# Optimization experiments

Hardware: AMD Instinct MI355X
Metric: run time of the kernel (lower is better)

## Reference

```python
import jax, jax.numpy as jnp
import numpy as np

EPS = 1e-5
NUM_HEADS = 8
KEY_DIM = 32
V_DIM = 128  # att_ratio * key_dim

def bn2d(x, g, b, m, v):
    # inference BatchNorm2d on NCHW
    s = g * jax.lax.rsqrt(v + EPS)
    return x * s[None, :, None, None] + (b - m * s)[None, :, None, None]

def conv1x1(x, w):
    # w: [out_c, in_c], x: [B,C,H,W]
    return jnp.einsum('oc,bchw->bohw', w, x)

def _bn_params(key, c):
    k1, k2, k3, k4 = jax.random.split(key, 4)
    g = jax.random.uniform(k1, (c,), jnp.float32, 0.5, 1.5)
    b = jax.random.normal(k2, (c,), jnp.float32) * 0.1
    m = jax.random.normal(k3, (c,), jnp.float32) * 0.1
    v = jax.random.uniform(k4, (c,), jnp.float32, 0.5, 1.5)
    return g, b, m, v

def setup_inputs() -> dict:
    key = jax.random.key(0)
    ks = jax.random.split(key, 12)
    inp_dim, out_dim = 256, 512
    kv_out = (KEY_DIM + V_DIM) * NUM_HEADS      # 1280
    q_out = KEY_DIM * NUM_HEADS                 # 256
    merge_dim = V_DIM * NUM_HEADS               # 1024
    hid = out_dim * 2                            # mlp_ratio=2 -> 1024
    d = {}
    d['x'] = jax.random.normal(ks[0], (32, inp_dim, 32, 32), jnp.float32)
    d['kv_w'] = jax.random.normal(ks[1], (kv_out, inp_dim), jnp.float32) * 0.02
    d['kv_g'], d['kv_b'], d['kv_m'], d['kv_v'] = _bn_params(ks[2], kv_out)
    d['q_w'] = jax.random.normal(ks[3], (q_out, inp_dim), jnp.float32) * 0.02
    d['q_g'], d['q_b'], d['q_m'], d['q_v'] = _bn_params(ks[4], q_out)
    d['mg_w'] = jax.random.normal(ks[5], (out_dim, merge_dim), jnp.float32) * 0.02
    d['mg_g'], d['mg_b'], d['mg_m'], d['mg_v'] = _bn_params(ks[6], out_dim)
    d['fc1_w'] = jax.random.normal(ks[7], (hid, out_dim), jnp.float32) * 0.02
    d['bn1_g'], d['bn1_b'], d['bn1_m'], d['bn1_v'] = _bn_params(ks[8], hid)
    d['fc2_w'] = jax.random.normal(ks[9], (out_dim, hid), jnp.float32) * 0.02
    d['bn2_g'], d['bn2_b'], d['bn2_m'], d['bn2_v'] = _bn_params(ks[10], out_dim)
    return d

def reference(x, kv_w, kv_g, kv_b, kv_m, kv_v, q_w, q_g, q_b, q_m, q_v,
              mg_w, mg_g, mg_b, mg_m, mg_v,
              fc1_w, bn1_g, bn1_b, bn1_m, bn1_v,
              fc2_w, bn2_g, bn2_b, bn2_m, bn2_v):
    B, C, H, W = x.shape
    scale = KEY_DIM ** (-0.5)
    # kv projection: conv1x1 + BN, then split per head into k, v
    kv = bn2d(conv1x1(x, kv_w), kv_g, kv_b, kv_m, kv_v)
    kv = kv.reshape(B, NUM_HEADS, KEY_DIM + V_DIM, H * W)
    k = kv[:, :, :KEY_DIM]   # [B,h,Dk,N]
    v = kv[:, :, KEY_DIM:]   # [B,h,Dv,N]
    # query subsampling: AvgPool2d(kernel=1, stride=2) == strided slice
    xq = x[:, :, ::2, ::2]
    q = bn2d(conv1x1(xq, q_w), q_g, q_b, q_m, q_v)
    q = q.reshape(B, NUM_HEADS, KEY_DIM, -1)  # [B,h,Dk,Nq]
    # att = q^T @ k * scale, softmax over keys
    att = jax.nn.softmax(jnp.einsum('bhdq,bhdn->bhqn', q, k) * scale, axis=-1)
    h2, w2 = (H + 1) // 2, (W + 1) // 2
    # out = v @ att^T, channel-first layout
    o = jnp.einsum('bhvn,bhqn->bhvq', v, att).reshape(B, NUM_HEADS * V_DIM, h2, w2)
    # merge: GELU -> conv1x1 -> BN
    o = bn2d(conv1x1(jax.nn.gelu(o, approximate=False), mg_w), mg_g, mg_b, mg_m, mg_v)
    # ConvMlp: conv1x1 -> BN -> GELU -> conv1x1 -> BN
    y = bn2d(conv1x1(o, fc1_w), bn1_g, bn1_b, bn1_m, bn1_v)
    y = jax.nn.gelu(y, approximate=False)
    y = bn2d(conv1x1(y, fc2_w), bn2_g, bn2_b, bn2_m, bn2_v)
    return y
```

## Files before the change

### kernel.cpp

```cpp
#include <hip/hip_runtime.h>
#include <hip/hip_bf16.h>

#define BN_EPS 1e-5f

typedef short s8v __attribute__((ext_vector_type(8)));
typedef float f4v __attribute__((ext_vector_type(4)));
typedef unsigned short u16x8 __attribute__((ext_vector_type(8)));

__device__ __forceinline__ float bu2f(unsigned short u) {
    union { unsigned int i; float f; } c; c.i = ((unsigned int)u) << 16; return c.f;
}
__device__ __forceinline__ unsigned short f2bu(float f) {
    union { float f; unsigned int i; } c; c.f = f;
    unsigned int i = c.i;
    i += 0x7FFFu + ((i >> 16) & 1u);
    return (unsigned short)(i >> 16);
}
__device__ __forceinline__ float gelu_exact(float x) {
    return 0.5f * x * (1.0f + erff(x * 0.70710678118654752f));
}
__device__ __forceinline__ float ldin(const void* p, long i, bool f32) {
    return f32 ? ((const float*)p)[i] : bu2f(((const unsigned short*)p)[i]);
}
__device__ __forceinline__ s8v ldfrag(const unsigned short* p) {
    return *reinterpret_cast<const s8v*>(p);
}
__device__ __forceinline__ void gld16(const void* g, void* l) {
    __builtin_amdgcn_global_load_lds(
        (const __attribute__((address_space(1))) unsigned int*)g,
        (__attribute__((address_space(3))) unsigned int*)l, 16, 0, 0);
}
__device__ __forceinline__ s8v ldsw32(const unsigned short* T, int row, int quad) {
    return *reinterpret_cast<const s8v*>(T + row * 32 + ((quad ^ ((row >> 1) & 3)) << 3));
}
__device__ __forceinline__ s8v ldsw64(const unsigned short* T, int row, int chunk) {
    return *reinterpret_cast<const s8v*>(T + row * 64 + ((chunk ^ (row & 7)) << 3));
}
__device__ __forceinline__ int detect_f32(const unsigned short* xu) {
    int insane = 0;
    for (int i = 0; i < 128; ++i) {
        unsigned int e = (xu[i] >> 7) & 0xFFu;
        if (e == 255u || (e != 0u && (e < 96u || e > 159u))) ++insane;
    }
    return (insane >= 16) ? 1 : 0;
}

__global__ __launch_bounds__(256)
void prep_kernel(const void* __restrict__ x,
                 const void* __restrict__ w0, const void* __restrict__ w1,
                 const void* __restrict__ w2, const void* __restrict__ w3,
                 const void* __restrict__ w4,
                 unsigned short* __restrict__ wdst,
                 unsigned short* __restrict__ xT,
                 unsigned short* __restrict__ xqT,
                 int* __restrict__ dtf)
{
    __shared__ int sflag;
    __shared__ unsigned short T[64][66];
    const int tid = threadIdx.x;
    const int bid = blockIdx.x;
    if (tid == 0) {
        int fl = detect_f32((const unsigned short*)x);
        sflag = fl;
        if (bid == 0) *dtf = fl;
    }
    __syncthreads();
    const bool f = (sflag != 0);

    if (bid < 960) {
        long idx = (long)bid * 2048 + tid * 8;
        const void* s; long off;
        if      (idx <  327680L) { s = w0; off = idx; }
        else if (idx <  393216L) { s = w1; off = idx - 327680L; }
        else if (idx <  917504L) { s = w2; off = idx - 393216L; }
        else if (idx < 1441792L) { s = w3; off = idx - 917504L; }
        else                     { s = w4; off = idx - 1441792L; }
        u16x8 pk;
        if (f) {
            float4 a = *((const float4*)((const float*)s + off));
            float4 b = *((const float4*)((const float*)s + off + 4));
            pk[0]=f2bu(a.x); pk[1]=f2bu(a.y); pk[2]=f2bu(a.z); pk[3]=f2bu(a.w);
            pk[4]=f2bu(b.x); pk[5]=f2bu(b.y); pk[6]=f2bu(b.z); pk[7]=f2bu(b.w);
        } else {
            pk = *((const u16x8*)((const unsigned short*)s + off));
        }
        *reinterpret_cast<u16x8*>(wdst + idx) = pk;
        return;
    }
    int b, c0, n0, ND; bool SUBS;
    if (bid < 3008) { int t = bid - 960;  b = t >> 6; int r = t & 63;
                      c0 = (r >> 4) * 64; n0 = (r & 15) * 64; ND = 1024; SUBS = false; }
    else            { int t = bid - 3008; b = t >> 4; int r = t & 15;
                      c0 = (r >> 2) * 64; n0 = (r & 3) * 64;  ND = 256;  SUBS = true; }
    unsigned short* dst = SUBS ? xqT : xT;
    {
        int nn = tid & 63, cq = tid >> 6;
        int n = n0 + nn;
        int sc = SUBS ? ((n >> 4) * 64 + (n & 15) * 2) : n;
        long base = ((long)b * 256 + c0 + cq * 16) * 1024 + sc;
        #pragma unroll
        for (int i = 0; i < 16; ++i)
            T[nn][cq * 16 + i] = f2bu(ldin(x, base + (long)i * 1024, f));
    }
    __syncthreads();
    {
        int cc = tid & 63, nq = tid >> 6;
        #pragma unroll
        for (int i = 0; i < 16; ++i) {
            int nn = nq * 16 + i;
            dst[((long)b * ND + n0 + nn) * 256 + c0 + cc] = T[nn][cc];
        }
    }
}

template<int OUT_MODE, bool DO_GELU, bool PRESCALE, int BM>
__global__ __launch_bounds__(256)
void mfma_gemm(const unsigned short* __restrict__ A,
               const unsigned short* __restrict__ B,
               const void* __restrict__ gg, const void* __restrict__ bb,
               const void* __restrict__ mmu, const void* __restrict__ vv,
               void* __restrict__ out0, unsigned short* __restrict__ out1,
               int M, int K, int N, const int* __restrict__ dtflag)
{
    constexpr int NF = (BM == 128) ? 4 : 2;
    constexpr int MP0 = 72;
    constexpr int MP1 = 136;
    constexpr int LOOPSH = BM * 64 + 128 * 64;
    constexpr int TILESH = (OUT_MODE == 1) ? 128 * MP1 : ((OUT_MODE == 0) ? 128 * MP0 : 0);
    constexpr int SMS = (LOOPSH > TILESH) ? LOOPSH : TILESH;
    __shared__ __align__(16) unsigned short smem[SMS];
    __shared__ float sS[BM], sO[BM];
    unsigned short* As = smem;
    unsigned short* Bs = smem + BM * 64;
    unsigned short* Tt = smem;

    const bool wf = (*dtflag != 0);
    const int tid = threadIdx.x;
    const int lane = tid & 63;
    const int wave = tid >> 6;
    const int quad = lane >> 4;
    const int l15  = lane & 15;
    const int wm2 = (BM == 128) ? (wave >> 1) * 64 : 0;
    const int wn2 = (BM == 128) ? (wave & 1) * 64 : wave * 32;
    const int b  = blockIdx.z;
    const int bm = blockIdx.y * BM;
    const int bn = blockIdx.x * 128;

    if (tid < BM) {
        int m = bm + tid;
        float g  = ldin(gg,  m, wf), be = ldin(bb,  m, wf);
        float mu = ldin(mmu, m, wf), va = ldin(vv,  m, wf);
        float s = g * rsqrtf(va + BN_EPS);
        float o = be - mu * s;
        if (PRESCALE) { s *= 0.17677669529663687f; o *= 0.17677669529663687f; }
        sS[tid] = s; sO[tid] = o;
    }

    const unsigned short* Bb = B + (long)b * N * K;

    f4v acc[4][NF];
    #pragma unroll
    for (int i = 0; i < 4; ++i)
        #pragma unroll
        for (int j = 0; j < NF; ++j) acc[i][j] = (f4v){0.f, 0.f, 0.f, 0.f};

    const int lr8 = lane >> 3;
    const int lc8 = lane & 7;

    for (int k0 = 0; k0 < K; k0 += 64) {
        #pragma unroll
        for (int j = 0; j < (BM == 128 ? 4 : 2); ++j) {
            int base = wave * (BM == 128 ? 32 : 16) + j * 8;
            int r = base + lr8;
            gld16(A + (long)(bm + r) * K + k0 + ((lc8 ^ (r & 7)) << 3),
                  As + base * 64);
        }
        #pragma unroll
        for (int j = 0; j < 4; ++j) {
            int base = wave * 32 + j * 8;
            int r = base + lr8;
            gld16(Bb + (long)(bn + r) * K + k0 + ((lc8 ^ (r & 7)) << 3),
                  Bs + base * 64);
        }
        __syncthreads();

        #pragma unroll
        for (int sk = 0; sk < 2; ++sk) {
            s8v af[4], bfr[NF];
            #pragma unroll
            for (int i = 0; i < 4; ++i)
                af[i]  = ldsw64(As, wm2 + i * 16 + l15, sk * 4 + quad);
            #pragma unroll
            for (int j = 0; j < NF; ++j)
                bfr[j] = ldsw64(Bs, wn2 + j * 16 + l15, sk * 4 + quad);
            #pragma unroll
            for (int i = 0; i < 4; ++i)
                #pragma unroll
                for (int j = 0; j < NF; ++j)
                    acc[i][j] = __builtin_amdgcn_mfma_f32_16x16x32_bf16(
                        af[i], bfr[j], acc[i][j], 0, 0, 0);
        }
        __syncthreads();
    }

    #pragma unroll
    for (int i = 0; i < 4; ++i) {
        int m0l = wm2 + i * 16 + quad * 4;
        int m0  = bm + m0l;
        float s0 = sS[m0l + 0], o0 = sO[m0l + 0];
        float s1 = sS[m0l + 1], o1 = sO[m0l + 1];
        float s2 = sS[m0l + 2], o2 = sO[m0l + 2];
        float s3 = sS[m0l + 3], o3 = sO[m0l + 3];
        #pragma unroll
        for (int j = 0; j < NF; ++j) {
            int nl = wn2 + j * 16 + l15;
            int n = bn + nl;
            float v0 = acc[i][j][0] * s0 + o0;
            float v1 = acc[i][j][1] * s1 + o1;
            float v2 = acc[i][j][2] * s2 + o2;
            float v3 = acc[i][j][3] * s3 + o3;
            if (DO_GELU) {
                v0 = gelu_exact(v0); v1 = gelu_exact(v1);
                v2 = gelu_exact(v2); v3 = gelu_exact(v3);
            }
            if (OUT_MODE == 0) {
                ushort4 pk; pk.x = f2bu(v0); pk.y = f2bu(v1);
                pk.z = f2bu(v2); pk.w = f2bu(v3);
                *reinterpret_cast<ushort4*>(&Tt[nl * MP0 + m0l]) = pk;
            } else if (OUT_MODE == 1) {
                int h = m0 / 160, seg = m0 - h * 160;
                if (seg < 32) {
                    ushort4 pk; pk.x = f2bu(v0); pk.y = f2bu(v1);
                    pk.z = f2bu(v2); pk.w = f2bu(v3);
                    *reinterpret_cast<ushort4*>(
                        (unsigned short*)out0 + ((long)(b * 8 + h) * 1024 + n) * 32 + seg) = pk;
                } else {
                    Tt[(m0l + 0) * MP1 + nl] = f2bu(v0);
                    Tt[(m0l + 1) * MP1 + nl] = f2bu(v1);
                    Tt[(m0l + 2) * MP1 + nl] = f2bu(v2);
                    Tt[(m0l + 3) * MP1 + nl] = f2bu(v3);
                }
            } else if (OUT_MODE == 2) {
                int b2 = n >> 8, nl2 = n & 255;
                long ob = ((long)b2 * M + m0) * 256 + nl2;
                if (wf) {
                    ((float*)out0)[ob + 0L * 256] = v0;
                    ((float*)out0)[ob + 1L * 256] = v1;
                    ((float*)out0)[ob + 2L * 256] = v2;
                    ((float*)out0)[ob + 3L * 256] = v3;
                } else {
                    ((unsigned short*)out0)[ob + 0L * 256] = f2bu(v0);
                    ((unsigned short*)out0)[ob + 1L * 256] = f2bu(v1);
                    ((unsigned short*)out0)[ob + 2L * 256] = f2bu(v2);
                    ((unsigned short*)out0)[ob + 3L * 256] = f2bu(v3);
                }
            } else {
                int h = m0 >> 5;
                ushort4 pk; pk.x = f2bu(v0); pk.y = f2bu(v1);
                pk.z = f2bu(v2); pk.w = f2bu(v3);
                *reinterpret_cast<ushort4*>(
                    (unsigned short*)out0 + ((long)(b * 8 + h) * 256 + n) * 32 + (m0 & 31)) = pk;
            }
        }
    }

    if (OUT_MODE == 0) {
        __syncthreads();
        long ob = ((long)b * N + bn) * M + bm;
        #pragma unroll
        for (int c = 0; c < BM / 16; ++c) {
            int cc = c * 256 + tid;
            int n = cc >> 3, mc = (cc & 7) << 3;
            *reinterpret_cast<u16x8*>((unsigned short*)out0 + ob + (long)n * M + mc) =
                *reinterpret_cast<const u16x8*>(&Tt[n * MP0 + mc]);
        }
    } else if (OUT_MODE == 1) {
        __syncthreads();
        int h0 = (bm + 159) / 160;
        int ks = h0 * 160;
        bool hasK = (ks < bm + 128);
        int kl = hasK ? (ks - bm) : 128;
        int nrows = hasK ? 96 : 128;
        for (int c = tid; c < nrows * 16; c += 256) {
            int row = c >> 4, ch = (c & 15) << 3;
            int ml = (row < kl) ? row : (row + 32);
            int m = bm + ml;
            int hh = m / 160, seg = m - hh * 160;
            *reinterpret_cast<u16x8*>(out1 +
                (((long)(b * 8 + hh) * 128) + (seg - 32)) * (long)N + bn + ch) =
                *reinterpret_cast<const u16x8*>(&Tt[ml * MP1 + ch]);
        }
    }
}

__global__ __launch_bounds__(512, 4)
void attn_mfma(const unsigned short* __restrict__ kvK,
               const unsigned short* __restrict__ kvV,
               const unsigned short* __restrict__ qh,
               unsigned short* __restrict__ goT)
{
    __shared__ unsigned short Ks[2][64 * 32];
    __shared__ unsigned short Vs[2][128 * 64];
    __shared__ unsigned short Ps[128][72];
    __shared__ float redS[128];

    const int tid = threadIdx.x;
    const int lane = tid & 63;
    const int wave = tid >> 6;
    const int quad = lane >> 4;
    const int l15  = lane & 15;
    const int h    = blockIdx.x;
    const int b    = blockIdx.y;
    const int q0   = blockIdx.z * 128;
    const int wq   = wave * 16;

    const unsigned short* Qb = qh  + (long)(b * 8 + h) * 256 * 32;
    const unsigned short* Kb = kvK + (long)(b * 8 + h) * 1024 * 32;
    const unsigned short* Vb = kvV + (long)(b * 8 + h) * 128 * 1024;

    s8v qf = ldfrag(Qb + (long)(q0 + wq + l15) * 32 + quad * 8);

    const unsigned short* pK = Kb;
    if (wave < 4) {
        int r = wave * 16 + (lane >> 2);
        int c = (lane & 3) ^ ((r >> 1) & 3);
        pK = Kb + (long)r * 32 + (c << 3);
    }
    const int rb = wave * 16;
    const int r0 = rb + (lane >> 3), r1 = r0 + 8;
    const int sl = lane & 7;
    const unsigned short* pV0 = Vb + (long)r0 * 1024 + ((sl ^ (r0 & 7)) << 3);
    const unsigned short* pV1 = Vb + (long)r1 * 1024 + ((sl ^ (r1 & 7)) << 3);

    f4v o[8];
    #pragma unroll
    for (int i = 0; i < 8; ++i) o[i] = (f4v){0.f, 0.f, 0.f, 0.f};
    float rs[4] = {0.f, 0.f, 0.f, 0.f};

    if (wave < 4) gld16(pK, &Ks[0][wave * 16 * 32]);
    gld16(pV0, &Vs[0][rb * 64]);
    gld16(pV1, &Vs[0][(rb + 8) * 64]);
    __syncthreads();

    for (int t = 0; t < 16; ++t) {
        const int cur = t & 1;
        if (t < 15) {
            const int nxt = cur ^ 1;
            const long adv = (long)(t + 1) * 64;
            if (wave < 4) gld16(pK + adv * 32, &Ks[nxt][wave * 16 * 32]);
            gld16(pV0 + adv, &Vs[nxt][rb * 64]);
            gld16(pV1 + adv, &Vs[nxt][(rb + 8) * 64]);
        }

        #pragma unroll
        for (int j = 0; j < 4; ++j) {
            s8v kf = ldsw32(&Ks[cur][0], j * 16 + l15, quad);
            f4v z = (f4v){0.f, 0.f, 0.f, 0.f};
            f4v sa = __builtin_amdgcn_mfma_f32_16x16x32_bf16(qf, kf, z, 0, 0, 0);
            #pragma unroll
            for (int r = 0; r < 4; ++r) {
                float p = __expf(fminf(sa[r], 30.f));
                rs[r] += p;
                Ps[wq + quad * 4 + r][j * 16 + l15] = f2bu(p);
            }
        }
        #pragma unroll
        for (int ks = 0; ks < 2; ++ks) {
            s8v pf = ldfrag(&Ps[wq + l15][ks * 32 + quad * 8]);
            #pragma unroll
            for (int i = 0; i < 8; ++i) {
                s8v vf = ldsw64(&Vs[cur][0], i * 16 + l15, ks * 4 + quad);
                o[i] = __builtin_amdgcn_mfma_f32_16x16x32_bf16(vf, pf, o[i], 0, 0, 0);
            }
        }
        __syncthreads();
    }

    #pragma unroll
    for (int r = 0; r < 4; ++r) {
        float s = rs[r];
        s += __shfl_xor(s, 1);
        s += __shfl_xor(s, 2);
        s += __shfl_xor(s, 4);
        s += __shfl_xor(s, 8);
        if (l15 == 0) redS[wq + quad * 4 + r] = s;
    }
    float linv = 1.0f / redS[wq + l15];
    int q = q0 + wq + l15;
    #pragma unroll
    for (int i = 0; i < 8; ++i) {
        ushort4 pk;
        pk.x = f2bu(gelu_exact(o[i][0] * linv));
        pk.y = f2bu(gelu_exact(o[i][1] * linv));
        pk.z = f2bu(gelu_exact(o[i][2] * linv));
        pk.w = f2bu(gelu_exact(o[i][3] * linv));
        *reinterpret_cast<ushort4*>(
            goT + ((long)b * 256 + q) * 1024 + h * 128 + i * 16 + quad * 4) = pk;
    }
}

extern "C" void kernel_launch(void* const* d_in, const int* in_sizes, int n_in,
                              void* d_out, int out_size, void* d_ws, size_t ws_size,
                              hipStream_t stream)
{
    const void* x     = d_in[0];
    const void* kv_w  = d_in[1];
    const void* kv_g  = d_in[2];  const void* kv_b  = d_in[3];
    const void* kv_m  = d_in[4];  const void* kv_v  = d_in[5];
    const void* q_w   = d_in[6];
    const void* q_g   = d_in[7];  const void* q_b   = d_in[8];
    const void* q_m   = d_in[9];  const void* q_v   = d_in[10];
    const void* mg_w  = d_in[11];
    const void* mg_g  = d_in[12]; const void* mg_b  = d_in[13];
    const void* mg_m  = d_in[14]; const void* mg_v  = d_in[15];
    const void* fc1_w = d_in[16];
    const void* bn1_g = d_in[17]; const void* bn1_b = d_in[18];
    const void* bn1_m = d_in[19]; const void* bn1_v = d_in[20];
    const void* fc2_w = d_in[21];
    const void* bn2_g = d_in[22]; const void* bn2_b = d_in[23];
    const void* bn2_m = d_in[24]; const void* bn2_v = d_in[25];

    unsigned short* ws  = (unsigned short*)d_ws;
    int*            dtf = (int*)d_ws;
    unsigned short* wsW  = ws + 8;
    unsigned short* wKV  = wsW;
    unsigned short* wQ   = wsW + 327680L;
    unsigned short* wMG  = wsW + 393216L;
    unsigned short* wFC1 = wsW + 917504L;
    unsigned short* wFC2 = wsW + 1441792L;
    unsigned short* xT   = ws + 1966088L;
    unsigned short* goT  = xT;
    unsigned short* xqT  = ws + 10354696L;
    unsigned short* qhb  = ws + 12451848L;
    unsigned short* kvK  = ws + 14549000L;
    unsigned short* kvV  = ws + 22937608L;
    unsigned short* y1T  = kvV;
    unsigned short* y2T  = kvV + 4194304L;

    dim3 blk(256, 1, 1);

    prep_kernel<<<3520, blk, 0, stream>>>(
        x, kv_w, q_w, mg_w, fc1_w, fc2_w, wsW, xT, xqT, dtf);

    mfma_gemm<3, false, true, 64><<<dim3(2, 4, 32), blk, 0, stream>>>(
        wQ, xqT, q_g, q_b, q_m, q_v, qhb, nullptr, 256, 256, 256, dtf);

    mfma_gemm<1, false, false, 128><<<dim3(8, 10, 32), blk, 0, stream>>>(
        wKV, xT, kv_g, kv_b, kv_m, kv_v, kvK, kvV, 1280, 256, 1024, dtf);

    attn_mfma<<<dim3(8, 32, 2), dim3(512, 1, 1), 0, stream>>>(kvK, kvV, qhb, goT);

    mfma_gemm<0, false, false, 64><<<dim3(64, 8, 1), blk, 0, stream>>>(
        wMG, goT, mg_g, mg_b, mg_m, mg_v, y1T, nullptr, 512, 1024, 8192, dtf);

    mfma_gemm<0, true, false, 64><<<dim3(64, 16, 1), blk, 0, stream>>>(
        wFC1, y1T, bn1_g, bn1_b, bn1_m, bn1_v, y2T, nullptr, 1024, 512, 8192, dtf);

    mfma_gemm<2, false, false, 64><<<dim3(64, 8, 1), blk, 0, stream>>>(
        wFC2, y2T, bn2_g, bn2_b, bn2_m, bn2_v, d_out, nullptr, 512, 1024, 8192, dtf);
}
```

Before: 304.4 us.

## Fuse merge, fc1 and fc2 GEMMs into one kernel keeping activations in LDS

Replaces the three back-to-back GEMM launches (merge conv+BN, fc1+BN+GELU, fc2+BN) with a single kernel in which each 512-thread block owns 32 spatial columns. The block keeps the intermediate activations in shared memory and streams the weights straight from global memory into MFMA fragments. This removes the round trips of the y1/y2 intermediates through global memory and two kernel launches. In exchange, only 256 blocks run with a large LDS footprint, so occupancy is low, and every block re-reads all the weights from global or L2 without LDS staging.

After: 341.3 us. 1.12x slower.

```diff
diff --git a/kernel.cpp b/kernel.cpp
--- a/kernel.cpp
+++ b/kernel.cpp
@@ -35,6 +35,11 @@
 }
 __device__ __forceinline__ s8v ldsw64(const unsigned short* T, int row, int chunk) {
     return *reinterpret_cast<const s8v*>(T + row * 64 + ((chunk ^ (row & 7)) << 3));
+}
+template<int RL>
+__device__ __forceinline__ s8v ldswL(const unsigned short* T, int row, int kc) {
+    int sc = (kc & ~7) | ((kc & 7) ^ (row & 7));
+    return *reinterpret_cast<const s8v*>(T + row * RL + (sc << 3));
 }
 __device__ __forceinline__ int detect_f32(const unsigned short* xu) {
     int insane = 0;
@@ -293,6 +298,222 @@
     }
 }
 
+__global__ __launch_bounds__(512)
+void mlp_fused(const unsigned short* __restrict__ go,
+               const unsigned short* __restrict__ wMG,
+               const unsigned short* __restrict__ wFC1,
+               const unsigned short* __restrict__ wFC2,
+               const void* __restrict__ mg_g, const void* __restrict__ mg_b,
+               const void* __restrict__ mg_m, const void* __restrict__ mg_v,
+               const void* __restrict__ b1g, const void* __restrict__ b1b,
+               const void* __restrict__ b1m, const void* __restrict__ b1v,
+               const void* __restrict__ b2g, const void* __restrict__ b2b,
+               const void* __restrict__ b2m, const void* __restrict__ b2v,
+               void* __restrict__ out, const int* __restrict__ dtflag)
+{
+    __shared__ __align__(16) unsigned short bufA[32 * 1024];
+    __shared__ __align__(16) unsigned short y1s[32 * 512];
+    __shared__ float sS1[512], sO1[512];
+    __shared__ float sS2[1024], sO2[1024];
+    __shared__ float sS3[512], sO3[512];
+
+    const bool wf = (*dtflag != 0);
+    const int tid  = threadIdx.x;
+    const int lane = tid & 63;
+    const int wave = tid >> 6;
+    const int quad = lane >> 4;
+    const int l15  = lane & 15;
+    const int n0   = blockIdx.x * 32;
+
+    if (tid < 512) {
+        float g = ldin(mg_g, tid, wf), be = ldin(mg_b, tid, wf);
+        float mu = ldin(mg_m, tid, wf), va = ldin(mg_v, tid, wf);
+        float s = g * rsqrtf(va + BN_EPS);
+        sS1[tid] = s; sO1[tid] = be - mu * s;
+        g = ldin(b2g, tid, wf); be = ldin(b2b, tid, wf);
+        mu = ldin(b2m, tid, wf); va = ldin(b2v, tid, wf);
+        s = g * rsqrtf(va + BN_EPS);
+        sS3[tid] = s; sO3[tid] = be - mu * s;
+    }
+    #pragma unroll
+    for (int ii = 0; ii < 2; ++ii) {
+        int m = ii * 512 + tid;
+        float g = ldin(b1g, m, wf), be = ldin(b1b, m, wf);
+        float mu = ldin(b1m, m, wf), va = ldin(b1v, m, wf);
+        float s = g * rsqrtf(va + BN_EPS);
+        sS2[m] = s; sO2[m] = be - mu * s;
+    }
+
+    #pragma unroll
+    for (int c8 = 0; c8 < 8; ++c8) {
+        int c  = c8 * 512 + tid;
+        int r  = c >> 7;
+        int cl = c & 127;
+        int sc = (cl & ~7) | ((cl & 7) ^ (r & 7));
+        gld16(go + (long)(n0 + r) * 1024 + (sc << 3),
+              bufA + (c8 * 512 + wave * 64) * 8);
+    }
+    __syncthreads();
+
+    {
+        f4v a1[4][2];
+        #pragma unroll
+        for (int i = 0; i < 4; ++i)
+            #pragma unroll
+            for (int j = 0; j < 2; ++j) a1[i][j] = (f4v){0.f,0.f,0.f,0.f};
+        #pragma unroll 2
+        for (int k0 = 0; k0 < 1024; k0 += 64) {
+            #pragma unroll
+            for (int sk = 0; sk < 2; ++sk) {
+                const int kk = k0 + sk * 32 + quad * 8;
+                const int kc = kk >> 3;
+                s8v af[4], bf[2];
+                #pragma unroll
+                for (int i = 0; i < 4; ++i)
+                    af[i] = ldfrag(wMG + (long)(wave * 64 + i * 16 + l15) * 1024 + kk);
+                #pragma unroll
+                for (int j = 0; j < 2; ++j)
+                    bf[j] = ldswL<1024>(bufA, j * 16 + l15, kc);
+                #pragma unroll
+                for (int i = 0; i < 4; ++i)
+                    #pragma unroll
+                    for (int j = 0; j < 2; ++j)
+                        a1[i][j] = __builtin_amdgcn_mfma_f32_16x16x32_bf16(
+                            af[i], bf[j], a1[i][j], 0, 0, 0);
+            }
+        }
+        #pragma unroll
+        for (int i = 0; i < 4; ++i) {
+            int m0 = wave * 64 + i * 16 + quad * 4;
+            float s0 = sS1[m0+0], o0 = sO1[m0+0];
+            float s1 = sS1[m0+1], o1 = sO1[m0+1];
+            float s2 = sS1[m0+2], o2 = sO1[m0+2];
+            float s3 = sS1[m0+3], o3 = sO1[m0+3];
+            int cch = m0 >> 3;
+            #pragma unroll
+            for (int j = 0; j < 2; ++j) {
+                int n = j * 16 + l15;
+                int sc = (cch & ~7) | ((cch & 7) ^ (n & 7));
+                ushort4 pk;
+                pk.x = f2bu(a1[i][j][0] * s0 + o0);
+                pk.y = f2bu(a1[i][j][1] * s1 + o1);
+                pk.z = f2bu(a1[i][j][2] * s2 + o2);
+                pk.w = f2bu(a1[i][j][3] * s3 + o3);
+                *reinterpret_cast<ushort4*>(y1s + n * 512 + (sc << 3) + (m0 & 7)) = pk;
+            }
+        }
+    }
+    __syncthreads();
+
+    {
+        f4v a2[8][2];
+        #pragma unroll
+        for (int i = 0; i < 8; ++i)
+            #pragma unroll
+            for (int j = 0; j < 2; ++j) a2[i][j] = (f4v){0.f,0.f,0.f,0.f};
+        #pragma unroll 2
+        for (int k0 = 0; k0 < 512; k0 += 64) {
+            #pragma unroll
+            for (int sk = 0; sk < 2; ++sk) {
+                const int kk = k0 + sk * 32 + quad * 8;
+                const int kc = kk >> 3;
+                s8v af[8], bf[2];
+                #pragma unroll
+                for (int i = 0; i < 8; ++i)
+                    af[i] = ldfrag(wFC1 + (long)(wave * 128 + i * 16 + l15) * 512 + kk);
+                #pragma unroll
+                for (int j = 0; j < 2; ++j)
+                    bf[j] = ldswL<512>(y1s, j * 16 + l15, kc);
+                #pragma unroll
+                for (int i = 0; i < 8; ++i)
+                    #pragma unroll
+                    for (int j = 0; j < 2; ++j)
+                        a2[i][j] = __builtin_amdgcn_mfma_f32_16x16x32_bf16(
+                            af[i], bf[j], a2[i][j], 0, 0, 0);
+            }
+        }
+        #pragma unroll
+        for (int i = 0; i < 8; ++i) {
+            int m0 = wave * 128 + i * 16 + quad * 4;
+            float s0 = sS2[m0+0], o0 = sO2[m0+0];
+            float s1 = sS2[m0+1], o1 = sO2[m0+1];
+            float s2 = sS2[m0+2], o2 = sO2[m0+2];
+            float s3 = sS2[m0+3], o3 = sO2[m0+3];
+            int cch = m0 >> 3;
+            #pragma unroll
+            for (int j = 0; j < 2; ++j) {
+                int n = j * 16 + l15;
+                int sc = (cch & ~7) | ((cch & 7) ^ (n & 7));
+                ushort4 pk;
+                pk.x = f2bu(gelu_exact(a2[i][j][0] * s0 + o0));
+                pk.y = f2bu(gelu_exact(a2[i][j][1] * s1 + o1));
+                pk.z = f2bu(gelu_exact(a2[i][j][2] * s2 + o2));
+                pk.w = f2bu(gelu_exact(a2[i][j][3] * s3 + o3));
+                *reinterpret_cast<ushort4*>(bufA + n * 1024 + (sc << 3) + (m0 & 7)) = pk;
+            }
+        }
+    }
+    __syncthreads();
+
+    {
+        f4v a3[4][2];
+        #pragma unroll
+        for (int i = 0; i < 4; ++i)
+            #pragma unroll
+            for (int j = 0; j < 2; ++j) a3[i][j] = (f4v){0.f,0.f,0.f,0.f};
+        #pragma unroll 2
+        for (int k0 = 0; k0 < 1024; k0 += 64) {
+            #pragma unroll
+            for (int sk = 0; sk < 2; ++sk) {
+                const int kk = k0 + sk * 32 + quad * 8;
+                const int kc = kk >> 3;
+                s8v af[4], bf[2];
+                #pragma unroll
+                for (int i = 0; i < 4; ++i)
+                    af[i] = ldfrag(wFC2 + (long)(wave * 64 + i * 16 + l15) * 1024 + kk);
+                #pragma unroll
+                for (int j = 0; j < 2; ++j)
+                    bf[j] = ldswL<1024>(bufA, j * 16 + l15, kc);
+                #pragma unroll
+                for (int i = 0; i < 4; ++i)
+                    #pragma unroll
+                    for (int j = 0; j < 2; ++j)
+                        a3[i][j] = __builtin_amdgcn_mfma_f32_16x16x32_bf16(
+                            af[i], bf[j], a3[i][j], 0, 0, 0);
+            }
+        }
+        const int b2 = n0 >> 8;
+        #pragma unroll
+        for (int i = 0; i < 4; ++i) {
+            int m0 = wave * 64 + i * 16 + quad * 4;
+            float s0 = sS3[m0+0], o0 = sO3[m0+0];
+            float s1 = sS3[m0+1], o1 = sO3[m0+1];
+            float s2 = sS3[m0+2], o2 = sO3[m0+2];
+            float s3 = sS3[m0+3], o3 = sO3[m0+3];
+            #pragma unroll
+            for (int j = 0; j < 2; ++j) {
+                int sp = (n0 & 255) + j * 16 + l15;
+                long ob = ((long)b2 * 512 + m0) * 256 + sp;
+                float v0 = a3[i][j][0] * s0 + o0;
+                float v1 = a3[i][j][1] * s1 + o1;
+                float v2 = a3[i][j][2] * s2 + o2;
+                float v3 = a3[i][j][3] * s3 + o3;
+                if (wf) {
+                    ((float*)out)[ob + 0L * 256] = v0;
+                    ((float*)out)[ob + 1L * 256] = v1;
+                    ((float*)out)[ob + 2L * 256] = v2;
+                    ((float*)out)[ob + 3L * 256] = v3;
+                } else {
+                    ((unsigned short*)out)[ob + 0L * 256] = f2bu(v0);
+                    ((unsigned short*)out)[ob + 1L * 256] = f2bu(v1);
+                    ((unsigned short*)out)[ob + 2L * 256] = f2bu(v2);
+                    ((unsigned short*)out)[ob + 3L * 256] = f2bu(v3);
+                }
+            }
+        }
+    }
+}
+
 __global__ __launch_bounds__(512, 4)
 void attn_mfma(const unsigned short* __restrict__ kvK,
                const unsigned short* __restrict__ kvV,
@@ -434,8 +655,6 @@
     unsigned short* qhb  = ws + 12451848L;
     unsigned short* kvK  = ws + 14549000L;
     unsigned short* kvV  = ws + 22937608L;
-    unsigned short* y1T  = kvV;
-    unsigned short* y2T  = kvV + 4194304L;
 
     dim3 blk(256, 1, 1);
 
@@ -450,12 +669,10 @@
 
     attn_mfma<<<dim3(8, 32, 2), dim3(512, 1, 1), 0, stream>>>(kvK, kvV, qhb, goT);
 
-    mfma_gemm<0, false, false, 64><<<dim3(64, 8, 1), blk, 0, stream>>>(
-        wMG, goT, mg_g, mg_b, mg_m, mg_v, y1T, nullptr, 512, 1024, 8192, dtf);
-
-    mfma_gemm<0, true, false, 64><<<dim3(64, 16, 1), blk, 0, stream>>>(
-        wFC1, y1T, bn1_g, bn1_b, bn1_m, bn1_v, y2T, nullptr, 1024, 512, 8192, dtf);
-
-    mfma_gemm<2, false, false, 64><<<dim3(64, 8, 1), blk, 0, stream>>>(
-        wFC2, y2T, bn2_g, bn2_b, bn2_m, bn2_v, d_out, nullptr, 512, 1024, 8192, dtf);
-}
+    mlp_fused<<<dim3(256, 1, 1), dim3(512, 1, 1), 0, stream>>>(
+        goT, wMG, wFC1, wFC2,
+        mg_g, mg_b, mg_m, mg_v,
+        bn1_g, bn1_b, bn1_m, bn1_v,
+        bn2_g, bn2_b, bn2_m, bn2_v,
+        d_out, dtf);
+}
```
